# Performance work log

Measured on AMD Instinct MI355X. Metric: run time of the kernel, lower is better.

The kernel has to match this reference:

```python
import jax, jax.numpy as jnp
import numpy as np

ALPHA = 0.2
BN_EPS = 1e-5
NEG = -9e15


def make_quaternion_mul(kernel):
    # kernel: [in/4, out]; split columns into quaternion components
    dim = kernel.shape[1] // 4
    r, i, j, k = jnp.split(kernel, 4, axis=1)
    r2 = jnp.concatenate([r, -i, -j, -k], axis=0)
    i2 = jnp.concatenate([i, r, -k, j], axis=0)
    j2 = jnp.concatenate([j, k, r, -i], axis=0)
    k2 = jnp.concatenate([k, -j, i, r], axis=0)
    return jnp.concatenate([r2, i2, j2, k2], axis=1)  # [in, out]


def setup_inputs() -> dict:
    key = jax.random.key(0)
    k1, k2, k3, k4 = jax.random.split(key, 4)
    N, IN, OUT = 8192, 512, 128
    inp = jax.random.normal(k1, (N, IN), dtype=jnp.float32)
    adj = jax.random.randint(k2, (N, N), 0, 2, dtype=jnp.int32)
    # xavier-like init for params
    W = jax.random.normal(k3, (IN // 4, OUT), dtype=jnp.float32) * (1.0 / np.sqrt(IN // 4))
    a = jax.random.normal(k4, (2 * OUT, 1), dtype=jnp.float32) * (1.0 / np.sqrt(2 * OUT))
    bn_gamma = jnp.ones((OUT,), dtype=jnp.float32)
    bn_beta = jnp.zeros((OUT,), dtype=jnp.float32)
    return {"input": inp, "adj": adj, "W": W, "a": a, "bn_gamma": bn_gamma, "bn_beta": bn_beta}


def reference(input, adj, W, a, bn_gamma, bn_beta):
    out_features = W.shape[1]
    hamilton = make_quaternion_mul(W)           # [in, out]
    h = input @ hamilton                        # [N, out]
    # a_input[i,j] = concat(h_i, h_j); a_input @ a decomposes as
    # (h @ a1)_i + (h @ a2)_j with a1 = a[:out], a2 = a[out:]
    a1 = a[:out_features, 0]                    # [out]
    a2 = a[out_features:, 0]                    # [out]
    s1 = h @ a1                                 # [N]
    s2 = h @ a2                                 # [N]
    e = s1[:, None] + s2[None, :]               # [N, N]
    e = jnp.where(e > 0, e, ALPHA * e)          # leaky_relu
    attention = jnp.where(adj > 0, e, NEG)
    attention = jax.nn.softmax(attention, axis=1)
    # dropout is identity in inference
    h_prime = attention @ h                     # [N, out]
    # BatchNorm1d (training-mode batch statistics, biased variance)
    mean = jnp.mean(h_prime, axis=0)
    var = jnp.var(h_prime, axis=0)
    h_prime = (h_prime - mean) / jnp.sqrt(var + BN_EPS) * bn_gamma + bn_beta
    # concat=True -> ELU
    return jax.nn.elu(h_prime)
```

## Files before the change

kernel.cpp:

```cpp
#include <hip/hip_runtime.h>
#include <hip/hip_bf16.h>
#include <math.h>

#define N_NODES 8192
#define IN_F    512
#define OUT_F   128
#define LRELU_A 0.2f
#define EPS_BN  1e-5f
#define MSH     40.0f
#define NSPLIT  8
#define JSPAN   (N_NODES / NSPLIT)
#define TILE_I  64

typedef unsigned short u16;
typedef unsigned int   u32;
typedef unsigned long long u64;
typedef __attribute__((ext_vector_type(8))) short  short8;
typedef __attribute__((ext_vector_type(4))) float  floatx4;

__device__ __forceinline__ u16 f2bf_rtn(float x) {
    u32 u = __float_as_uint(x);
    return (u16)((u + 0x7fffu + ((u >> 16) & 1u)) >> 16);
}

__global__ __launch_bounds__(256) void k_hamT(const float* __restrict__ W, u16* __restrict__ hamT,
                                              float* __restrict__ s1, float* __restrict__ s2,
                                              float* __restrict__ cs, float* __restrict__ cq) {
    const int idx = blockIdx.x * 256 + threadIdx.x;
    if (idx < N_NODES) { s1[idx] = 0.f; s2[idx] = 0.f; }
    if (idx < OUT_F)   { cs[idx] = 0.f; cq[idx] = 0.f; }
    const int c = idx >> 9, k = idx & 511;
    const int b = c >> 5, cc = c & 31, p = k >> 7, q = k & 127;
    const u32 NEGMASK = 0x284Eu;
    const float sg = ((NEGMASK >> (b * 4 + p)) & 1u) ? -1.f : 1.f;
    hamT[idx] = f2bf_rtn(sg * W[q * 128 + (b ^ p) * 32 + cc]);
}

__global__ __launch_bounds__(256) void k_h(const float* __restrict__ inp, const u16* __restrict__ hamT,
                                           const float* __restrict__ a,
                                           u16* __restrict__ hT, float* __restrict__ s1, float* __restrict__ s2) {
    __shared__ float red[4][128][20];
    const int t = threadIdx.x;
    const int lane = t & 63, wid = t >> 6;
    const int quad = lane >> 4, n = lane & 15;
    const int i0 = blockIdx.x * 16;
    const int kb = wid * 128;

    floatx4 acc[8];
#pragma unroll
    for (int ct = 0; ct < 8; ++ct) acc[ct] = (floatx4){0.f, 0.f, 0.f, 0.f};

#pragma unroll
    for (int ks = 0; ks < 4; ++ks) {
        const float* ap = inp + (size_t)(i0 + n) * IN_F + kb + ks * 32 + quad * 8;
        float4 a0 = *(const float4*)ap;
        float4 a1 = *(const float4*)(ap + 4);
        union { u32 u[4]; short8 s; } fa;
        fa.u[0] = (u32)f2bf_rtn(a0.x) | ((u32)f2bf_rtn(a0.y) << 16);
        fa.u[1] = (u32)f2bf_rtn(a0.z) | ((u32)f2bf_rtn(a0.w) << 16);
        fa.u[2] = (u32)f2bf_rtn(a1.x) | ((u32)f2bf_rtn(a1.y) << 16);
        fa.u[3] = (u32)f2bf_rtn(a1.z) | ((u32)f2bf_rtn(a1.w) << 16);
#pragma unroll
        for (int ct = 0; ct < 8; ++ct) {
            short8 fb = *(const short8*)&hamT[(ct * 16 + n) * IN_F + kb + ks * 32 + quad * 8];
            acc[ct] = __builtin_amdgcn_mfma_f32_16x16x32_bf16(fa.s, fb, acc[ct], 0, 0, 0);
        }
    }

    {
        float p1[4] = {0.f, 0.f, 0.f, 0.f}, p2[4] = {0.f, 0.f, 0.f, 0.f};
#pragma unroll
        for (int ct = 0; ct < 8; ++ct) {
            const int c = ct * 16 + n;
            const float a1v = a[c], a2v = a[OUT_F + c];
#pragma unroll
            for (int r = 0; r < 4; ++r) { p1[r] += acc[ct][r] * a1v; p2[r] += acc[ct][r] * a2v; }
        }
#pragma unroll
        for (int m = 1; m < 16; m <<= 1) {
#pragma unroll
            for (int r = 0; r < 4; ++r) {
                p1[r] += __shfl_xor(p1[r], m, 64);
                p2[r] += __shfl_xor(p2[r], m, 64);
            }
        }
        if (n == 0) {
#pragma unroll
            for (int r = 0; r < 4; ++r) {
                atomicAdd(&s1[i0 + quad * 4 + r], p1[r]);
                atomicAdd(&s2[i0 + quad * 4 + r], p2[r]);
            }
        }
    }

#pragma unroll
    for (int ct = 0; ct < 8; ++ct)
        *(float4*)&red[wid][ct * 16 + n][quad * 4] = *(float4*)&acc[ct];
    __syncthreads();

    {
        const int c = t >> 1, ih = (t & 1) * 8;
        float v[8];
#pragma unroll
        for (int e = 0; e < 8; ++e)
            v[e] = red[0][c][ih + e] + red[1][c][ih + e] + red[2][c][ih + e] + red[3][c][ih + e];
        uint4 pk;
        pk.x = (u32)f2bf_rtn(v[0]) | ((u32)f2bf_rtn(v[1]) << 16);
        pk.y = (u32)f2bf_rtn(v[2]) | ((u32)f2bf_rtn(v[3]) << 16);
        pk.z = (u32)f2bf_rtn(v[4]) | ((u32)f2bf_rtn(v[5]) << 16);
        pk.w = (u32)f2bf_rtn(v[6]) | ((u32)f2bf_rtn(v[7]) << 16);
        *(uint4*)&hT[(size_t)c * N_NODES + i0 + ih] = pk;
    }
}

__global__ __launch_bounds__(256, 4) void k_att(const int* __restrict__ adj, const u16* __restrict__ hT,
                                                const float* __restrict__ s1, const float* __restrict__ s2,
                                                float* __restrict__ Opart, float* __restrict__ Lpart) {
    __shared__ u16 hs[2][128 * 64];
    const int t = threadIdx.x;
    const int lane = t & 63, wid = t >> 6;
    const int quad = lane >> 4, n = lane & 15;
    const int i0 = blockIdx.x * TILE_I;
    const int jbase = blockIdx.y * JSPAN;
    const int i_lane = i0 + wid * 16 + n;
    const float s1v = s1[i_lane];
    const int scr = t >> 3, scj = (t & 7) * 8;

    u32 M[4][8];
#pragma unroll
    for (int g = 0; g < 4; ++g)
#pragma unroll
        for (int w = 0; w < 8; ++w) M[g][w] = 0u;
    {
        const size_t rowbase = (size_t)(i0 + wid * 16);
#pragma unroll 4
        for (int rr = 0; rr < 16; ++rr) {
            const int* ap = adj + (rowbase + rr) * N_NODES + jbase + lane * 4;
            uint4 v[4];
#pragma unroll
            for (int g = 0; g < 4; ++g) v[g] = *(const uint4*)(ap + g * 256);
            const bool kp = (n == rr);
#pragma unroll
            for (int g = 0; g < 4; ++g) {
                u64 c0 = __ballot((int)v[g].x > 0);
                u64 c1 = __ballot((int)v[g].y > 0);
                u64 c2 = __ballot((int)v[g].z > 0);
                u64 c3 = __ballot((int)v[g].w > 0);
                if (kp) {
                    M[g][0] = (u32)c0; M[g][1] = (u32)(c0 >> 32);
                    M[g][2] = (u32)c1; M[g][3] = (u32)(c1 >> 32);
                    M[g][4] = (u32)c2; M[g][5] = (u32)(c2 >> 32);
                    M[g][6] = (u32)c3; M[g][7] = (u32)(c3 >> 32);
                }
            }
        }
    }

#pragma unroll
    for (int ps = 0; ps < 4; ++ps) {
        const int cr = ps * 32 + scr;
        uint4 v = *(const uint4*)&hT[(size_t)cr * N_NODES + jbase + scj];
        *(uint4*)&hs[0][cr * 64 + (scj ^ ((cr & 7) * 8))] = v;
    }
    __syncthreads();

    floatx4 acc[8];
#pragma unroll
    for (int ct = 0; ct < 8; ct++) acc[ct] = (floatx4){0.f, 0.f, 0.f, 0.f};
    float Lacc = 0.f;

#pragma unroll
    for (int g = 0; g < 4; ++g) {
#pragma unroll
        for (int chi = 0; chi < 4; ++chi) {
            const int ch = g * 4 + chi;
            const int cur = ch & 1;
            const bool more = (ch + 1 < 16);
            uint4 H[4];
            if (more) {
#pragma unroll
                for (int ps = 0; ps < 4; ++ps) {
                    const int cr = ps * 32 + scr;
                    H[ps] = *(const uint4*)&hT[(size_t)cr * N_NODES + jbase + (ch + 1) * 64 + scj];
                }
            }
            short8 fa[2];
#pragma unroll
            for (int ks = 0; ks < 2; ++ks) {
                const float* s2p = s2 + jbase + ch * 64 + ks * 32 + quad * 8;
                float4 sa = *(const float4*)s2p;
                float4 sb = *(const float4*)(s2p + 4);
                const float sv[8] = {sa.x, sa.y, sa.z, sa.w, sb.x, sb.y, sb.z, sb.w};
                union { u32 u[4]; short8 s; } cv;
#pragma unroll
                for (int jh = 0; jh < 4; ++jh) {
                    float w2[2];
#pragma unroll
                    for (int e = 0; e < 2; ++e) {
                        const int jj = jh * 2 + e;
                        const u32 word = M[g][(jj & 3) * 2 + (chi >> 1)];
                        const int sh = (chi & 1) * 16 + ks * 8 + quad * 2 + (jj >> 2);
                        const u32 mbit = (word >> sh) & 1u;
                        float sc = s1v + sv[jj];
                        sc = fmaxf(sc, LRELU_A * sc);
                        float w = mbit ? __expf(sc - MSH) : 0.f;
                        Lacc += w;
                        w2[e] = w;
                    }
                    cv.u[jh] = (u32)f2bf_rtn(w2[0]) | ((u32)f2bf_rtn(w2[1]) << 16);
                }
                fa[ks] = cv.s;
            }
#pragma unroll
            for (int ct = 0; ct < 8; ++ct) {
                const int rb = ct * 16 + n;
                const int sw = (rb & 7) * 8;
                short8 fb0 = *(const short8*)&hs[cur][rb * 64 + ((quad * 8) ^ sw)];
                short8 fb1 = *(const short8*)&hs[cur][rb * 64 + ((32 + quad * 8) ^ sw)];
                acc[ct] = __builtin_amdgcn_mfma_f32_16x16x32_bf16(fa[0], fb0, acc[ct], 0, 0, 0);
                acc[ct] = __builtin_amdgcn_mfma_f32_16x16x32_bf16(fa[1], fb1, acc[ct], 0, 0, 0);
            }
            if (more) {
#pragma unroll
                for (int ps = 0; ps < 4; ++ps) {
                    const int cr = ps * 32 + scr;
                    *(uint4*)&hs[cur ^ 1][cr * 64 + (scj ^ ((cr & 7) * 8))] = H[ps];
                }
            }
            __syncthreads();
        }
    }

    Lacc += __shfl_xor(Lacc, 16, 64);
    Lacc += __shfl_xor(Lacc, 32, 64);
    if (lane < 16)
        Lpart[(size_t)blockIdx.y * N_NODES + i_lane] = Lacc;

    const size_t obase = (size_t)blockIdx.y * N_NODES * OUT_F;
#pragma unroll
    for (int ct = 0; ct < 8; ++ct) {
#pragma unroll
        for (int r = 0; r < 4; ++r) {
            const int i = i0 + wid * 16 + quad * 4 + r;
            Opart[obase + (size_t)i * OUT_F + ct * 16 + n] = acc[ct][r];
        }
    }
}

__global__ __launch_bounds__(256) void k_comb(const float* __restrict__ Opart, const float* __restrict__ Lpart,
                                              float* __restrict__ hp, float* __restrict__ cs, float* __restrict__ cq) {
    const int t = threadIdx.x;
    const int c = t & 127, half = t >> 7;
    const int ibase = blockIdx.x * 16;
    float sv = 0.f, sq = 0.f;
    for (int k = 0; k < 8; k++) {
        const int i = ibase + half + (k << 1);
        float o = 0.f, L = 0.f;
#pragma unroll
        for (int s = 0; s < NSPLIT; s++) {
            o += Opart[((size_t)s * N_NODES + i) * OUT_F + c];
            L += Lpart[(size_t)s * N_NODES + i];
        }
        float v = L > 0.f ? o / L : 0.f;
        hp[(size_t)i * OUT_F + c] = v;
        sv += v; sq += v * v;
    }
    __shared__ float red[256];
    red[t] = sv; __syncthreads();
    if (half == 0) atomicAdd(&cs[c], sv + red[t + 128]);
    __syncthreads(); red[t] = sq; __syncthreads();
    if (half == 0) atomicAdd(&cq[c], sq + red[t + 128]);
}

__global__ __launch_bounds__(256) void k_bn(const float* __restrict__ hp, const float* __restrict__ cs,
                                            const float* __restrict__ cq, const float* __restrict__ gamma,
                                            const float* __restrict__ beta, float* __restrict__ out) {
    const int idx = blockIdx.x * 256 + threadIdx.x;
    const int c = idx & 127;
    const float mean = cs[c] * (1.f / N_NODES);
    const float var  = cq[c] * (1.f / N_NODES) - mean * mean;
    float x = (hp[idx] - mean) * rsqrtf(var + EPS_BN) * gamma[c] + beta[c];
    x = x > 0.f ? x : expm1f(x);
    out[idx] = x;
}

extern "C" void kernel_launch(void* const* d_in, const int* in_sizes, int n_in,
                              void* d_out, int out_size, void* d_ws, size_t ws_size,
                              hipStream_t stream) {
    (void)in_sizes; (void)n_in; (void)out_size; (void)ws_size;
    const float* inp   = (const float*)d_in[0];
    const int*   adj   = (const int*)d_in[1];
    const float* W     = (const float*)d_in[2];
    const float* a     = (const float*)d_in[3];
    const float* gamma = (const float*)d_in[4];
    const float* beta  = (const float*)d_in[5];
    float* out = (float*)d_out;

    char* wsb = (char*)d_ws;
    u16*   hamT = (u16*)wsb;   wsb += (size_t)OUT_F * IN_F * 2;
    u16*   hT   = (u16*)wsb;   wsb += (size_t)OUT_F * N_NODES * 2;
    float* s1   = (float*)wsb; wsb += N_NODES * 4;
    float* s2   = (float*)wsb; wsb += N_NODES * 4;
    float* Op   = (float*)wsb; wsb += (size_t)NSPLIT * N_NODES * OUT_F * 4;
    float* Lp   = (float*)wsb; wsb += (size_t)NSPLIT * N_NODES * 4;
    float* hp   = (float*)wsb; wsb += (size_t)N_NODES * OUT_F * 4;
    float* cs   = (float*)wsb; wsb += OUT_F * 4;
    float* cq   = (float*)wsb; wsb += OUT_F * 4;

    hipLaunchKernelGGL(k_hamT, dim3(256), dim3(256), 0, stream, W, hamT, s1, s2, cs, cq);
    hipLaunchKernelGGL(k_h,    dim3(512), dim3(256), 0, stream, inp, hamT, a, hT, s1, s2);
    hipLaunchKernelGGL(k_att,  dim3(128, NSPLIT), dim3(256), 0, stream, adj, hT, s1, s2, Op, Lp);
    hipLaunchKernelGGL(k_comb, dim3(512), dim3(256), 0, stream, Op, Lp, hp, cs, cq);
    hipLaunchKernelGGL(k_bn,   dim3(4096), dim3(256), 0, stream, hp, cs, cq, gamma, beta, out);
}
```

Baseline: 455.0 us.

## Stage inputs in LDS, fragment-order Hamilton weights, cache s2, coarsen combine

The input tile for k_h is now converted to bf16 once and staged in padded shared memory, so global reads are coalesced. The Hamilton matrix is stored in MFMA fragment order so each B-fragment load is contiguous. k_att copies its s2 span into shared memory instead of re-reading global memory per chunk. k_comb processes 64 rows per block with a quarter of the blocks, which cuts the number of atomics. These are several independent memory-access tweaks, and the shared memory added to k_h and k_att may reduce occupancy.

```diff
diff --git a/kernel.cpp b/kernel.cpp
--- a/kernel.cpp
+++ b/kernel.cpp
@@ -11,6 +11,7 @@
 #define NSPLIT  8
 #define JSPAN   (N_NODES / NSPLIT)
 #define TILE_I  64
+#define ISTR    520
 
 typedef unsigned short u16;
 typedef unsigned int   u32;
@@ -23,22 +24,24 @@
     return (u16)((u + 0x7fffu + ((u >> 16) & 1u)) >> 16);
 }
 
-__global__ __launch_bounds__(256) void k_hamT(const float* __restrict__ W, u16* __restrict__ hamT,
+__global__ __launch_bounds__(256) void k_hamT(const float* __restrict__ W, u16* __restrict__ hamF,
                                               float* __restrict__ s1, float* __restrict__ s2,
                                               float* __restrict__ cs, float* __restrict__ cq) {
     const int idx = blockIdx.x * 256 + threadIdx.x;
     if (idx < N_NODES) { s1[idx] = 0.f; s2[idx] = 0.f; }
     if (idx < OUT_F)   { cs[idx] = 0.f; cq[idx] = 0.f; }
     const int c = idx >> 9, k = idx & 511;
-    const int b = c >> 5, cc = c & 31, p = k >> 7, q = k & 127;
+    const int b = c >> 5, cc = c & 31, kp = k >> 7, kq = k & 127;
     const u32 NEGMASK = 0x284Eu;
-    const float sg = ((NEGMASK >> (b * 4 + p)) & 1u) ? -1.f : 1.f;
-    hamT[idx] = f2bf_rtn(sg * W[q * 128 + (b ^ p) * 32 + cc]);
-}
-
-__global__ __launch_bounds__(256) void k_h(const float* __restrict__ inp, const u16* __restrict__ hamT,
+    const float sg = ((NEGMASK >> (b * 4 + kp)) & 1u) ? -1.f : 1.f;
+    const int kappa = k >> 5, q = (k >> 3) & 3, e = k & 7;
+    hamF[((kappa * 4 + q) * 128 + c) * 8 + e] = f2bf_rtn(sg * W[kq * 128 + (b ^ kp) * 32 + cc]);
+}
+
+__global__ __launch_bounds__(256) void k_h(const float* __restrict__ inp, const u16* __restrict__ hamF,
                                            const float* __restrict__ a,
                                            u16* __restrict__ hT, float* __restrict__ s1, float* __restrict__ s2) {
+    __shared__ u16 inA[16 * ISTR];
     __shared__ float red[4][128][20];
     const int t = threadIdx.x;
     const int lane = t & 63, wid = t >> 6;
@@ -46,24 +49,28 @@
     const int i0 = blockIdx.x * 16;
     const int kb = wid * 128;
 
+#pragma unroll
+    for (int u = 0; u < 8; ++u) {
+        float4 v = *(const float4*)&inp[(size_t)i0 * IN_F + u * 1024 + t * 4];
+        const int r = u * 2 + (t >> 7);
+        const int col = (t & 127) * 4;
+        u64 pk = (u64)f2bf_rtn(v.x) | ((u64)f2bf_rtn(v.y) << 16)
+               | ((u64)f2bf_rtn(v.z) << 32) | ((u64)f2bf_rtn(v.w) << 48);
+        *(u64*)&inA[r * ISTR + col] = pk;
+    }
+    __syncthreads();
+
     floatx4 acc[8];
 #pragma unroll
     for (int ct = 0; ct < 8; ++ct) acc[ct] = (floatx4){0.f, 0.f, 0.f, 0.f};
 
 #pragma unroll
     for (int ks = 0; ks < 4; ++ks) {
-        const float* ap = inp + (size_t)(i0 + n) * IN_F + kb + ks * 32 + quad * 8;
-        float4 a0 = *(const float4*)ap;
-        float4 a1 = *(const float4*)(ap + 4);
-        union { u32 u[4]; short8 s; } fa;
-        fa.u[0] = (u32)f2bf_rtn(a0.x) | ((u32)f2bf_rtn(a0.y) << 16);
-        fa.u[1] = (u32)f2bf_rtn(a0.z) | ((u32)f2bf_rtn(a0.w) << 16);
-        fa.u[2] = (u32)f2bf_rtn(a1.x) | ((u32)f2bf_rtn(a1.y) << 16);
-        fa.u[3] = (u32)f2bf_rtn(a1.z) | ((u32)f2bf_rtn(a1.w) << 16);
+        short8 fa = *(const short8*)&inA[n * ISTR + kb + ks * 32 + quad * 8];
 #pragma unroll
         for (int ct = 0; ct < 8; ++ct) {
-            short8 fb = *(const short8*)&hamT[(ct * 16 + n) * IN_F + kb + ks * 32 + quad * 8];
-            acc[ct] = __builtin_amdgcn_mfma_f32_16x16x32_bf16(fa.s, fb, acc[ct], 0, 0, 0);
+            short8 fb = *(const short8*)&hamF[((wid * 4 + ks) * 4 + quad) * 1024 + (ct * 16 + n) * 8];
+            acc[ct] = __builtin_amdgcn_mfma_f32_16x16x32_bf16(fa, fb, acc[ct], 0, 0, 0);
         }
     }
 
@@ -117,6 +124,7 @@
                                                 const float* __restrict__ s1, const float* __restrict__ s2,
                                                 float* __restrict__ Opart, float* __restrict__ Lpart) {
     __shared__ u16 hs[2][128 * 64];
+    __shared__ float s2s[JSPAN];
     const int t = threadIdx.x;
     const int lane = t & 63, wid = t >> 6;
     const int quad = lane >> 4, n = lane & 15;
@@ -125,6 +133,8 @@
     const int i_lane = i0 + wid * 16 + n;
     const float s1v = s1[i_lane];
     const int scr = t >> 3, scj = (t & 7) * 8;
+
+    *(float4*)&s2s[t * 4] = *(const float4*)&s2[jbase + t * 4];
 
     u32 M[4][8];
 #pragma unroll
@@ -187,9 +197,9 @@
             short8 fa[2];
 #pragma unroll
             for (int ks = 0; ks < 2; ++ks) {
-                const float* s2p = s2 + jbase + ch * 64 + ks * 32 + quad * 8;
-                float4 sa = *(const float4*)s2p;
-                float4 sb = *(const float4*)(s2p + 4);
+                const int jl = ch * 64 + ks * 32 + quad * 8;
+                float4 sa = *(const float4*)&s2s[jl];
+                float4 sb = *(const float4*)&s2s[jl + 4];
                 const float sv[8] = {sa.x, sa.y, sa.z, sa.w, sb.x, sb.y, sb.z, sb.w};
                 union { u32 u[4]; short8 s; } cv;
 #pragma unroll
@@ -251,9 +261,9 @@
                                               float* __restrict__ hp, float* __restrict__ cs, float* __restrict__ cq) {
     const int t = threadIdx.x;
     const int c = t & 127, half = t >> 7;
-    const int ibase = blockIdx.x * 16;
+    const int ibase = blockIdx.x * 64;
     float sv = 0.f, sq = 0.f;
-    for (int k = 0; k < 8; k++) {
+    for (int k = 0; k < 32; k++) {
         const int i = ibase + half + (k << 1);
         float o = 0.f, L = 0.f;
 #pragma unroll
@@ -297,7 +307,7 @@
     float* out = (float*)d_out;
 
     char* wsb = (char*)d_ws;
-    u16*   hamT = (u16*)wsb;   wsb += (size_t)OUT_F * IN_F * 2;
+    u16*   hamF = (u16*)wsb;   wsb += (size_t)OUT_F * IN_F * 2;
     u16*   hT   = (u16*)wsb;   wsb += (size_t)OUT_F * N_NODES * 2;
     float* s1   = (float*)wsb; wsb += N_NODES * 4;
     float* s2   = (float*)wsb; wsb += N_NODES * 4;
@@ -307,9 +317,9 @@
     float* cs   = (float*)wsb; wsb += OUT_F * 4;
     float* cq   = (float*)wsb; wsb += OUT_F * 4;
 
-    hipLaunchKernelGGL(k_hamT, dim3(256), dim3(256), 0, stream, W, hamT, s1, s2, cs, cq);
-    hipLaunchKernelGGL(k_h,    dim3(512), dim3(256), 0, stream, inp, hamT, a, hT, s1, s2);
+    hipLaunchKernelGGL(k_hamT, dim3(256), dim3(256), 0, stream, W, hamF, s1, s2, cs, cq);
+    hipLaunchKernelGGL(k_h,    dim3(512), dim3(256), 0, stream, inp, hamF, a, hT, s1, s2);
     hipLaunchKernelGGL(k_att,  dim3(128, NSPLIT), dim3(256), 0, stream, adj, hT, s1, s2, Op, Lp);
-    hipLaunchKernelGGL(k_comb, dim3(512), dim3(256), 0, stream, Op, Lp, hp, cs, cq);
+    hipLaunchKernelGGL(k_comb, dim3(128), dim3(256), 0, stream, Op, Lp, hp, cs, cq);
     hipLaunchKernelGGL(k_bn,   dim3(4096), dim3(256), 0, stream, hp, cs, cq, gamma, beta, out);
 }
```

New measurement: 447.3 us. Within noise of the previous version (-1.7%).
